# Kernel optimization log

Hardware: AMD Instinct MI355X
Metric: run time of the kernel (lower is better)

Reference implementation:

```python
import jax, jax.numpy as jnp
import numpy as np

B, T, IN, H, OUT = 128, 1024, 17, 512, 17


def setup_inputs() -> dict:
    key = jax.random.key(0)
    ks = jax.random.split(key, 11)
    s_in = 1.0 / np.sqrt(H)
    return {
        "x": jax.random.normal(ks[0], (B, T, IN), dtype=jnp.float32),
        "wih0": jax.random.normal(ks[1], (4 * H, IN), dtype=jnp.float32) * s_in,
        "whh0": jax.random.normal(ks[2], (4 * H, H), dtype=jnp.float32) * s_in,
        "bih0": jax.random.normal(ks[3], (4 * H,), dtype=jnp.float32) * s_in,
        "bhh0": jax.random.normal(ks[4], (4 * H,), dtype=jnp.float32) * s_in,
        "wih1": jax.random.normal(ks[5], (4 * H, H), dtype=jnp.float32) * s_in,
        "whh1": jax.random.normal(ks[6], (4 * H, H), dtype=jnp.float32) * s_in,
        "bih1": jax.random.normal(ks[7], (4 * H,), dtype=jnp.float32) * s_in,
        "bhh1": jax.random.normal(ks[8], (4 * H,), dtype=jnp.float32) * s_in,
        "lin_w": jax.random.normal(ks[9], (OUT, H), dtype=jnp.float32) * s_in,
        "lin_b": jax.random.normal(ks[10], (OUT,), dtype=jnp.float32) * s_in,
    }


def _lstm_layer(x, wih, whh, bih, bhh):
    # x: [B, T, D]; gate order i, f, g, o (torch.nn.LSTMCell convention)
    b, _, _ = x.shape
    h = whh.shape[1]
    # Precompute input projection for all timesteps: [B, T, 4H]
    proj = jnp.einsum("btd,gd->btg", x, wih) + bih

    def step(carry, p_t):
        h_t, c_t = carry
        gates = p_t + h_t @ whh.T + bhh  # [B, 4H]
        i, f, g, o = jnp.split(gates, 4, axis=1)
        i = jax.nn.sigmoid(i)
        f = jax.nn.sigmoid(f)
        o = jax.nn.sigmoid(o)
        g = jnp.tanh(g)
        c_t = f * c_t + i * g
        h_t = o * jnp.tanh(c_t)
        return (h_t, c_t), h_t

    h0 = jnp.zeros((b, h), x.dtype)
    c0 = jnp.zeros((b, h), x.dtype)
    _, ys = jax.lax.scan(step, (h0, c0), jnp.swapaxes(proj, 0, 1))  # ys: [T, B, H]
    return jnp.swapaxes(ys, 0, 1)  # [B, T, H]


def reference(x, wih0, whh0, bih0, bhh0, wih1, whh1, bih1, bhh1, lin_w, lin_b):
    y = _lstm_layer(x, wih0, whh0, bih0, bhh0)
    y = _lstm_layer(y, wih1, whh1, bih1, bhh1)
    h_last = y[:, -1, :]  # [B, H]
    return h_last @ lin_w.T + lin_b  # [B, OUT]
```

## Files before the change

### kernel.cpp

```cpp
#include <hip/hip_runtime.h>
#include <cstddef>
#include <cstdint>

typedef unsigned long long ull;
typedef unsigned short u16;
typedef unsigned int u32;
typedef __attribute__((ext_vector_type(8))) short s8v;
typedef __attribute__((ext_vector_type(4))) float f4v;

#define GROUPS 8
#define BG     16
#define JS     16
#define TPB    256
#define NT     1024
#define HDIM   512
#define INDIM  17
#define OUTDIM 17
#define BTOT   128

#define AT_LD(p)   __hip_atomic_load((p), __ATOMIC_RELAXED, __HIP_MEMORY_SCOPE_AGENT)
#define AT_ST(p,v) __hip_atomic_store((p), (v), __ATOMIC_RELAXED, __HIP_MEMORY_SCOPE_AGENT)

#define PLANE32 8192
#define WIDX(k, b) ((((k) >> 5) * 512) + ((((k) >> 3) & 3) * 128) + ((b) * 8) + ((k) & 7))
#define SLICE(wg)  (((wg) >> 1) * 512 + ((wg) & 1) * 256)

#define RA_OFF     ((size_t)0)
#define RING_BYTES ((size_t)4 * GROUPS * PLANE32 * 4)
#define RB_OFF     (RA_OFF + RING_BYTES)
#define FB32_OFF   (RB_OFF + RING_BYTES)
#define WS_NEEDED  (FB32_OFF + (size_t)BTOT * HDIM * 4)
#define RIX32(sl, gr) (((size_t)(sl) * GROUPS + (gr)) * PLANE32)

#define L_H0   0
#define L_H1   49152
#define L_EXA  65536
#define L_EXB  69632
#define L_HOA  73728
#define L_HOB  74752
#define L_CTL  75776
#define LDS_SZ 75840

__device__ __forceinline__ u16 f2bf(float f) {
  unsigned int u = __float_as_uint(f);
  u += 0x7FFFu + ((u >> 16) & 1u);
  return (u16)(u >> 16);
}
__device__ __forceinline__ float bf2f(u16 h) {
  return __uint_as_float(((unsigned int)h) << 16);
}
__device__ __forceinline__ float sigm(float x) { return 1.f / (1.f + __expf(-x)); }
__device__ __forceinline__ float tanh_f(float x) { return 2.f / (1.f + __expf(-2.f * x)) - 1.f; }

#define MFMA(a, b, c) __builtin_amdgcn_mfma_f32_16x16x32_bf16((a), (b), (c), 0, 0, 0)

__device__ __forceinline__ void pbar(int* c, int& nbar, int lane) {
  ++nbar;
  if (lane == 0)
    (void)__hip_atomic_fetch_add(c, 1, __ATOMIC_RELEASE, __HIP_MEMORY_SCOPE_WORKGROUP);
  while (__hip_atomic_load(c, __ATOMIC_ACQUIRE, __HIP_MEMORY_SCOPE_WORKGROUP) < 2 * nbar) {}
}

__global__ __launch_bounds__(TPB, 1) void lstm_fused(
    const float* __restrict__ x,
    const float* __restrict__ wih0, const float* __restrict__ whh0,
    const float* __restrict__ bih0, const float* __restrict__ bhh0,
    const float* __restrict__ wih1, const float* __restrict__ whh1,
    const float* __restrict__ bih1, const float* __restrict__ bhh1,
    u32* __restrict__ ringA, u32* __restrict__ ringB,
    float* __restrict__ fb32)
{
  const int bid  = blockIdx.x;
  const int gr   = bid & 7;
  const int wg   = bid >> 3;
  const int j0   = wg * JS;
  const int tid  = threadIdx.x;
  const int wave = tid >> 6;
  const int lane = tid & 63;
  const int n    = lane & 15;
  const int q    = lane >> 4;
  const int k0   = q * 8;

  __shared__ __align__(16) char smem[LDS_SZ];
  int* ctl = (int*)(smem + L_CTL);
  float* exgA = (float*)(smem + L_EXA);
  float* exgB = (float*)(smem + L_EXB);

  if (tid < 8) ctl[tid] = 0;

  {
    int b_l = tid >> 4, j_l = tid & 15, jg = j0 + j_l;
    int wo = WIDX(jg, b_l);
    AT_ST(&ringA[RIX32(0, gr) + wo], 0u);
    AT_ST(&ringB[RIX32(0, gr) + wo], 0u);
  }
  __syncthreads();

  const f4v z = {0.f, 0.f, 0.f, 0.f};
  const int p  = (wave & 1) * 64 + lane;
  const int jq = p & 15, b0 = p >> 4;
  const int jg = j0 + jq;
  const int ho0 = (jq >> 3) * 128 + b0 * 8 + (jq & 7);
  const int ho1 = (jq >> 3) * 128 + (b0 + 8) * 8 + (jq & 7);
  const int slice = SLICE(wg);
  const int half = wave & 1;
  const ull TMASK = 0xFFFF0000FFFF0000ULL;

  if (wave < 2) {
    const int g0 = wave * 2;
    s8v wx_h[2], wx_l[2];
#pragma unroll
    for (int i = 0; i < 2; ++i) {
      const float* wr = wih0 + (size_t)((g0 + i) * HDIM + j0 + n) * INDIM;
#pragma unroll
      for (int j = 0; j < 8; ++j) {
        int k = k0 + j;
        float v = (k < INDIM) ? wr[k] : 0.f;
        u16 hi = f2bf(v);
        wx_h[i][j] = (short)hi;
        wx_l[i][j] = (short)f2bf(v - bf2f(hi));
      }
    }
    s8v wh_h[2][16], wh_l[2][16];
#pragma unroll
    for (int i = 0; i < 2; ++i) {
      const float* wr = whh0 + (size_t)((g0 + i) * HDIM + j0 + n) * HDIM;
#pragma unroll
      for (int kt = 0; kt < 16; ++kt)
#pragma unroll
        for (int j = 0; j < 8; ++j) {
          float v = wr[kt * 32 + k0 + j];
          u16 hi = f2bf(v);
          wh_h[i][kt][j] = (short)hi;
          wh_l[i][kt][j] = (short)f2bf(v - bf2f(hi));
        }
    }
    float bias[4];
#pragma unroll
    for (int g = 0; g < 4; ++g) bias[g] = bih0[g * HDIM + jg] + bhh0[g * HDIM + jg];
    float c0a = 0.f, c0b = 0.f;
    int nbar = 0;

    for (int s = 1; s <= NT + 1; ++s) {
      f4v xa[2] = {z, z};
      if (s <= NT) {
        const float* xr = x + ((size_t)(gr * BG + n) * NT + (s - 1)) * INDIM;
        s8v axh, axl;
#pragma unroll
        for (int j = 0; j < 8; ++j) {
          int k = k0 + j;
          float v = (k < INDIM) ? xr[k] : 0.f;
          u16 hi = f2bf(v);
          axh[j] = (short)hi;
          axl[j] = (short)f2bf(v - bf2f(hi));
        }
#pragma unroll
        for (int i = 0; i < 2; ++i) {
          xa[i] = MFMA(axh, wx_h[i], xa[i]);
          xa[i] = MFMA(axl, wx_h[i], xa[i]);
          xa[i] = MFMA(axh, wx_l[i], xa[i]);
        }
      }
      const int sl3 = (s - 1) % 3;
      {
        const ull* src = (const ull*)(ringA + RIX32((s - 1) & 3, gr)) + half * 2048;
        const ull tg = (ull)(u16)(s - 1);
        const ull pat = (tg << 16) | (tg << 48);
        ull v[32];
        for (;;) {
          ull acc = 0;
#pragma unroll
          for (int i = 0; i < 16; ++i) {
            v[2 * i]     = AT_LD(src + (i * 64 + lane) * 2);
            v[2 * i + 1] = AT_LD(src + (i * 64 + lane) * 2 + 1);
          }
#pragma unroll
          for (int i = 0; i < 32; ++i) acc |= (v[i] ^ pat) & TMASK;
          int l1t = __hip_atomic_load(&ctl[7], __ATOMIC_ACQUIRE,
                                      __HIP_MEMORY_SCOPE_WORKGROUP);
          if (__ballot(acc == 0) == ~0ULL && l1t >= s - 4) break;
          __builtin_amdgcn_s_sleep(1);
        }
        char* dst = smem + L_H0 + sl3 * 16384 + half * 8192;
#pragma unroll
        for (int i = 0; i < 16; ++i) {
          ull a = v[2 * i], b = v[2 * i + 1];
          ull packed = (a & 0xFFFFULL) | ((a >> 16) & 0xFFFF0000ULL)
                     | ((b & 0xFFFFULL) << 32) | (((b >> 16) & 0xFFFF0000ULL) << 32);
          *(ull*)(dst + (i * 64 + lane) * 8) = packed;
        }
      }
      pbar(&ctl[0], nbar, lane);
      if (wave == 0 && lane == 0)
        __hip_atomic_store(&ctl[4 + sl3], s - 1, __ATOMIC_RELEASE,
                           __HIP_MEMORY_SCOPE_WORKGROUP);
      if (s == NT + 1) break;

      const char* sh = smem + L_H0 + sl3 * 16384;
      f4v cHH[2] = {z, z}, cHL[2] = {z, z};
#pragma unroll
      for (int kt = 0; kt < 16; ++kt) {
        s8v ah = *(const s8v*)(sh + kt * 1024 + q * 256 + n * 16);
#pragma unroll
        for (int i = 0; i < 2; ++i) {
          cHH[i] = MFMA(ah, wh_h[i][kt], cHH[i]);
          cHL[i] = MFMA(ah, wh_l[i][kt], cHL[i]);
        }
      }
#pragma unroll
      for (int i = 0; i < 2; ++i) {
        f4v e = xa[i] + cHH[i] + cHL[i];
#pragma unroll
        for (int r = 0; r < 4; ++r)
          exgA[(g0 + i) * 256 + (q * 4 + r) * 16 + n] = e[r];
      }
      pbar(&ctl[0], nbar, lane);
      u32* ho = (u32*)(smem + L_HOA);
      const u32 otag = ((u32)(u16)s) << 16;
      {
        float pi = exgA[0 * 256 + b0 * 16 + jq] + bias[0];
        float pf = exgA[1 * 256 + b0 * 16 + jq] + bias[1];
        float pg = exgA[2 * 256 + b0 * 16 + jq] + bias[2];
        float po = exgA[3 * 256 + b0 * 16 + jq] + bias[3];
        float ig = sigm(pi), fg = sigm(pf), gg = tanh_f(pg), og = sigm(po);
        c0a = fg * c0a + ig * gg;
        ho[ho0] = otag | (u32)f2bf(og * tanh_f(c0a));
      }
      {
        float pi = exgA[0 * 256 + (b0 + 8) * 16 + jq] + bias[0];
        float pf = exgA[1 * 256 + (b0 + 8) * 16 + jq] + bias[1];
        float pg = exgA[2 * 256 + (b0 + 8) * 16 + jq] + bias[2];
        float po = exgA[3 * 256 + (b0 + 8) * 16 + jq] + bias[3];
        float ig = sigm(pi), fg = sigm(pf), gg = tanh_f(pg), og = sigm(po);
        c0b = fg * c0b + ig * gg;
        ho[ho1] = otag | (u32)f2bf(og * tanh_f(c0b));
      }
      pbar(&ctl[0], nbar, lane);
      {
        ull v0 = *(const ull*)(smem + L_HOA + (half * 64 + lane) * 8);
        ull* d = (ull*)(ringA + RIX32(s & 3, gr) + slice);
        AT_ST(d + half * 64 + lane, v0);
      }
    }
  } else {
    const int g0 = (wave - 2) * 2;
    s8v w1x[2][16], w1h[2][16];
#pragma unroll
    for (int i = 0; i < 2; ++i) {
      const float* p1 = wih1 + (size_t)((g0 + i) * HDIM + j0 + n) * HDIM;
      const float* p2 = whh1 + (size_t)((g0 + i) * HDIM + j0 + n) * HDIM;
#pragma unroll
      for (int kt = 0; kt < 16; ++kt)
#pragma unroll
        for (int j = 0; j < 8; ++j) {
          w1x[i][kt][j] = (short)f2bf(p1[kt * 32 + k0 + j]);
          w1h[i][kt][j] = (short)f2bf(p2[kt * 32 + k0 + j]);
        }
    }
    float bias[4];
#pragma unroll
    for (int g = 0; g < 4; ++g) bias[g] = bih1[g * HDIM + jg] + bhh1[g * HDIM + jg];
    float c1a = 0.f, c1b = 0.f;
    int nbar = 0;

    for (int t = 1; t <= NT; ++t) {
      {
        const ull* src = (const ull*)(ringB + RIX32((t - 1) & 3, gr)) + half * 2048;
        const ull tg = (ull)(u16)(t - 1);
        const ull pat = (tg << 16) | (tg << 48);
        ull v[32];
        for (;;) {
          ull acc = 0;
#pragma unroll
          for (int i = 0; i < 16; ++i) {
            v[2 * i]     = AT_LD(src + (i * 64 + lane) * 2);
            v[2 * i + 1] = AT_LD(src + (i * 64 + lane) * 2 + 1);
          }
#pragma unroll
          for (int i = 0; i < 32; ++i) acc |= (v[i] ^ pat) & TMASK;
          if (__ballot(acc == 0) == ~0ULL) break;
          __builtin_amdgcn_s_sleep(1);
        }
        char* dst = smem + L_H1 + half * 8192;
#pragma unroll
        for (int i = 0; i < 16; ++i) {
          ull a = v[2 * i], b = v[2 * i + 1];
          ull packed = (a & 0xFFFFULL) | ((a >> 16) & 0xFFFF0000ULL)
                     | ((b & 0xFFFFULL) << 32) | (((b >> 16) & 0xFFFF0000ULL) << 32);
          *(ull*)(dst + (i * 64 + lane) * 8) = packed;
        }
      }
      pbar(&ctl[1], nbar, lane);
      const char* th = smem + L_H1;
      f4v dHH[2] = {z, z};
#pragma unroll
      for (int kt = 0; kt < 16; ++kt) {
        s8v ah = *(const s8v*)(th + kt * 1024 + q * 256 + n * 16);
#pragma unroll
        for (int i = 0; i < 2; ++i) dHH[i] = MFMA(ah, w1h[i][kt], dHH[i]);
      }
      const int sl3 = t % 3;
      while (__hip_atomic_load(&ctl[4 + sl3], __ATOMIC_ACQUIRE,
                               __HIP_MEMORY_SCOPE_WORKGROUP) < t) {}
      const char* sh = smem + L_H0 + sl3 * 16384;
      f4v eHH[2] = {z, z};
#pragma unroll
      for (int kt = 0; kt < 16; ++kt) {
        s8v ah = *(const s8v*)(sh + kt * 1024 + q * 256 + n * 16);
#pragma unroll
        for (int i = 0; i < 2; ++i) eHH[i] = MFMA(ah, w1x[i][kt], eHH[i]);
      }
#pragma unroll
      for (int i = 0; i < 2; ++i) {
        f4v e = dHH[i] + eHH[i];
#pragma unroll
        for (int r = 0; r < 4; ++r)
          exgB[(g0 + i) * 256 + (q * 4 + r) * 16 + n] = e[r];
      }
      pbar(&ctl[1], nbar, lane);
      u32* ho = (u32*)(smem + L_HOB);
      const u32 otag = ((u32)(u16)t) << 16;
      {
        float pi = exgB[0 * 256 + b0 * 16 + jq] + bias[0];
        float pf = exgB[1 * 256 + b0 * 16 + jq] + bias[1];
        float pg = exgB[2 * 256 + b0 * 16 + jq] + bias[2];
        float po = exgB[3 * 256 + b0 * 16 + jq] + bias[3];
        float ig = sigm(pi), fg = sigm(pf), gg = tanh_f(pg), og = sigm(po);
        c1a = fg * c1a + ig * gg;
        float h = og * tanh_f(c1a);
        ho[ho0] = otag | (u32)f2bf(h);
        if (t == NT)
          AT_ST((u32*)&fb32[(size_t)(gr * BG + b0) * HDIM + jg], __float_as_uint(h));
      }
      {
        float pi = exgB[0 * 256 + (b0 + 8) * 16 + jq] + bias[0];
        float pf = exgB[1 * 256 + (b0 + 8) * 16 + jq] + bias[1];
        float pg = exgB[2 * 256 + (b0 + 8) * 16 + jq] + bias[2];
        float po = exgB[3 * 256 + (b0 + 8) * 16 + jq] + bias[3];
        float ig = sigm(pi), fg = sigm(pf), gg = tanh_f(pg), og = sigm(po);
        c1b = fg * c1b + ig * gg;
        float h = og * tanh_f(c1b);
        ho[ho1] = otag | (u32)f2bf(h);
        if (t == NT)
          AT_ST((u32*)&fb32[(size_t)(gr * BG + b0 + 8) * HDIM + jg], __float_as_uint(h));
      }
      pbar(&ctl[1], nbar, lane);
      {
        ull v0 = *(const ull*)(smem + L_HOB + (half * 64 + lane) * 8);
        ull* d = (ull*)(ringB + RIX32(t & 3, gr) + slice);
        AT_ST(d + half * 64 + lane, v0);
      }
      if (wave == 2 && lane == 0)
        __hip_atomic_store(&ctl[7], t, __ATOMIC_RELEASE,
                           __HIP_MEMORY_SCOPE_WORKGROUP);
    }
  }
}

__global__ void final_linear(const float* __restrict__ fb32,
                             const float* __restrict__ lin_w,
                             const float* __restrict__ lin_b,
                             float* __restrict__ out) {
  int b = blockIdx.x, o = threadIdx.x;
  if (o < OUTDIM) {
    float acc = lin_b[o];
    const u32* hr = (const u32*)(fb32 + (size_t)b * HDIM);
    for (int j = 0; j < HDIM; ++j) {
      float h = __uint_as_float(AT_LD(hr + j));
      acc += h * lin_w[(size_t)o * HDIM + j];
    }
    out[b * OUTDIM + o] = acc;
  }
}

__global__ void sentinel_kernel(float* __restrict__ out, int nv) {
  int i = blockIdx.x * TPB + threadIdx.x;
  if (i < nv) out[i] = 1e30f;
}

extern "C" void kernel_launch(void* const* d_in, const int* in_sizes, int n_in,
                              void* d_out, int out_size, void* d_ws, size_t ws_size,
                              hipStream_t stream) {
  (void)in_sizes; (void)n_in;
  const float* x     = (const float*)d_in[0];
  const float* wih0  = (const float*)d_in[1];
  const float* whh0  = (const float*)d_in[2];
  const float* bih0  = (const float*)d_in[3];
  const float* bhh0  = (const float*)d_in[4];
  const float* wih1  = (const float*)d_in[5];
  const float* whh1  = (const float*)d_in[6];
  const float* bih1  = (const float*)d_in[7];
  const float* bhh1  = (const float*)d_in[8];
  const float* lin_w = (const float*)d_in[9];
  const float* lin_b = (const float*)d_in[10];
  float* out = (float*)d_out;
  char* ws = (char*)d_ws;

  if (ws_size < WS_NEEDED) {
    sentinel_kernel<<<(out_size + TPB - 1) / TPB, TPB, 0, stream>>>(out, out_size);
    return;
  }

  u32* ringA  = (u32*)(ws + RA_OFF);
  u32* ringB  = (u32*)(ws + RB_OFF);
  float* fb32 = (float*)(ws + FB32_OFF);

  lstm_fused<<<256, TPB, 0, stream>>>(x, wih0, whh0, bih0, bhh0,
                                      wih1, whh1, bih1, bhh1,
                                      ringA, ringB, fb32);
  final_linear<<<BTOT, 64, 0, stream>>>(fb32, lin_w, lin_b, out);
}
```

Baseline: 4.733 ms.

## Store LSTM outputs directly to global ring and poll a sentinel before full load

Each thread now writes its tagged bf16 hidden value straight to the global ring with an atomic store. This removes the LDS staging buffer and one workgroup barrier per timestep in both layers. Consumers first spin on one sampled 64-bit word per lane before loading the full 32-word block, which cuts polling traffic. The costs are scattered 4-byte global stores instead of coalesced 8-byte ones, and an extra round of polling latency. LDS_SZ also grows to 81920.

```diff
diff --git a/kernel.cpp b/kernel.cpp
--- a/kernel.cpp
+++ b/kernel.cpp
@@ -36,10 +36,8 @@
 #define L_H1   49152
 #define L_EXA  65536
 #define L_EXB  69632
-#define L_HOA  73728
-#define L_HOB  74752
-#define L_CTL  75776
-#define LDS_SZ 75840
+#define L_CTL  73728
+#define LDS_SZ 81920
 
 __device__ __forceinline__ u16 f2bf(float f) {
   unsigned int u = __float_as_uint(f);
@@ -104,6 +102,7 @@
   const int ho1 = (jq >> 3) * 128 + (b0 + 8) * 8 + (jq & 7);
   const int slice = SLICE(wg);
   const int half = wave & 1;
+  const int sub = (lane >> 2) * 128 + (lane & 3) * 32;
   const ull TMASK = 0xFFFF0000FFFF0000ULL;
 
   if (wave < 2) {
@@ -166,6 +165,13 @@
         const ull* src = (const ull*)(ringA + RIX32((s - 1) & 3, gr)) + half * 2048;
         const ull tg = (ull)(u16)(s - 1);
         const ull pat = (tg << 16) | (tg << 48);
+        for (;;) {
+          ull w = AT_LD(src + sub);
+          int l1t = __hip_atomic_load(&ctl[7], __ATOMIC_ACQUIRE,
+                                      __HIP_MEMORY_SCOPE_WORKGROUP);
+          if (__ballot((((w ^ pat) & TMASK) == 0) & (l1t >= s - 4)) == ~0ULL) break;
+          __builtin_amdgcn_s_sleep(1);
+        }
         ull v[32];
         for (;;) {
           ull acc = 0;
@@ -176,9 +182,7 @@
           }
 #pragma unroll
           for (int i = 0; i < 32; ++i) acc |= (v[i] ^ pat) & TMASK;
-          int l1t = __hip_atomic_load(&ctl[7], __ATOMIC_ACQUIRE,
-                                      __HIP_MEMORY_SCOPE_WORKGROUP);
-          if (__ballot(acc == 0) == ~0ULL && l1t >= s - 4) break;
+          if (__ballot(acc == 0) == ~0ULL) break;
           __builtin_amdgcn_s_sleep(1);
         }
         char* dst = smem + L_H0 + sl3 * 16384 + half * 8192;
@@ -215,8 +219,8 @@
           exgA[(g0 + i) * 256 + (q * 4 + r) * 16 + n] = e[r];
       }
       pbar(&ctl[0], nbar, lane);
-      u32* ho = (u32*)(smem + L_HOA);
       const u32 otag = ((u32)(u16)s) << 16;
+      u32* d = (u32*)(ringA + RIX32(s & 3, gr) + slice);
       {
         float pi = exgA[0 * 256 + b0 * 16 + jq] + bias[0];
         float pf = exgA[1 * 256 + b0 * 16 + jq] + bias[1];
@@ -224,7 +228,7 @@
         float po = exgA[3 * 256 + b0 * 16 + jq] + bias[3];
         float ig = sigm(pi), fg = sigm(pf), gg = tanh_f(pg), og = sigm(po);
         c0a = fg * c0a + ig * gg;
-        ho[ho0] = otag | (u32)f2bf(og * tanh_f(c0a));
+        AT_ST(d + ho0, otag | (u32)f2bf(og * tanh_f(c0a)));
       }
       {
         float pi = exgA[0 * 256 + (b0 + 8) * 16 + jq] + bias[0];
@@ -233,13 +237,7 @@
         float po = exgA[3 * 256 + (b0 + 8) * 16 + jq] + bias[3];
         float ig = sigm(pi), fg = sigm(pf), gg = tanh_f(pg), og = sigm(po);
         c0b = fg * c0b + ig * gg;
-        ho[ho1] = otag | (u32)f2bf(og * tanh_f(c0b));
-      }
-      pbar(&ctl[0], nbar, lane);
-      {
-        ull v0 = *(const ull*)(smem + L_HOA + (half * 64 + lane) * 8);
-        ull* d = (ull*)(ringA + RIX32(s & 3, gr) + slice);
-        AT_ST(d + half * 64 + lane, v0);
+        AT_ST(d + ho1, otag | (u32)f2bf(og * tanh_f(c0b)));
       }
     }
   } else {
@@ -268,6 +266,11 @@
         const ull* src = (const ull*)(ringB + RIX32((t - 1) & 3, gr)) + half * 2048;
         const ull tg = (ull)(u16)(t - 1);
         const ull pat = (tg << 16) | (tg << 48);
+        for (;;) {
+          ull w = AT_LD(src + sub);
+          if (__ballot(((w ^ pat) & TMASK) == 0) == ~0ULL) break;
+          __builtin_amdgcn_s_sleep(1);
+        }
         ull v[32];
         for (;;) {
           ull acc = 0;
@@ -318,8 +321,8 @@
           exgB[(g0 + i) * 256 + (q * 4 + r) * 16 + n] = e[r];
       }
       pbar(&ctl[1], nbar, lane);
-      u32* ho = (u32*)(smem + L_HOB);
       const u32 otag = ((u32)(u16)t) << 16;
+      u32* d = (u32*)(ringB + RIX32(t & 3, gr) + slice);
       {
         float pi = exgB[0 * 256 + b0 * 16 + jq] + bias[0];
         float pf = exgB[1 * 256 + b0 * 16 + jq] + bias[1];
@@ -328,7 +331,7 @@
         float ig = sigm(pi), fg = sigm(pf), gg = tanh_f(pg), og = sigm(po);
         c1a = fg * c1a + ig * gg;
         float h = og * tanh_f(c1a);
-        ho[ho0] = otag | (u32)f2bf(h);
+        AT_ST(d + ho0, otag | (u32)f2bf(h));
         if (t == NT)
           AT_ST((u32*)&fb32[(size_t)(gr * BG + b0) * HDIM + jg], __float_as_uint(h));
       }
@@ -340,15 +343,9 @@
         float ig = sigm(pi), fg = sigm(pf), gg = tanh_f(pg), og = sigm(po);
         c1b = fg * c1b + ig * gg;
         float h = og * tanh_f(c1b);
-        ho[ho1] = otag | (u32)f2bf(h);
+        AT_ST(d + ho1, otag | (u32)f2bf(h));
         if (t == NT)
           AT_ST((u32*)&fb32[(size_t)(gr * BG + b0 + 8) * HDIM + jg], __float_as_uint(h));
-      }
-      pbar(&ctl[1], nbar, lane);
-      {
-        ull v0 = *(const ull*)(smem + L_HOB + (half * 64 + lane) * 8);
-        ull* d = (ull*)(ringB + RIX32(t & 3, gr) + slice);
-        AT_ST(d + half * 64 + lane, v0);
       }
       if (wave == 2 && lane == 0)
         __hip_atomic_store(&ctl[7], t, __ATOMIC_RELEASE,
```

New measurement: 4.641 ms. Within noise of the previous version (-1.9%).
